# Optimization experiments

Hardware: AMD Instinct MI355X
Metric: run time of the kernel (lower is better)

Reference implementation:

```python
import jax, jax.numpy as jnp
import numpy as np


def reference(x, coef_ref, coef_qry):
    # x: [B, Hr, Wr, Hq, Wq] similarity tensor
    B, Hr, Wr, Hq, Wq = x.shape
    xr = x.reshape(B, Hr * Wr, Hq * Wq)  # [B, R, Q]
    # softmax over ref axis (axis=1) of coef_ref * (x - max over axis 1)
    xm_ref = xr - jnp.max(xr, axis=1, keepdims=True)
    conf_ref = jax.nn.softmax(coef_ref[0] * xm_ref, axis=1)
    # softmax over qry axis (axis=2) of coef_qry * (x - max over axis 2)
    xm_qry = xr - jnp.max(xr, axis=2, keepdims=True)
    conf_qry = jax.nn.softmax(coef_qry[0] * xm_qry, axis=2)
    confidence = jnp.sqrt(conf_ref * conf_qry)  # [B, R, Q]
    # top_k(k=1) over last axis + gather_nd of that value == max over axis 2
    values = jnp.max(confidence, axis=2)  # [B, R]
    return values.reshape(B, Hr, Wr, 1)


def setup_inputs() -> dict:
    key = jax.random.key(0)
    k1, = jax.random.split(key, 1)
    B, Hr, Wr, Hq, Wq = 16, 64, 64, 32, 32
    alpha = 10.0
    x = jax.random.normal(k1, (B, Hr, Wr, Hq, Wq), dtype=jnp.float32)
    coef_ref = jnp.full((1,), alpha, dtype=jnp.float32)
    coef_qry = jnp.full((1,), alpha, dtype=jnp.float32)
    return {"x": x, "coef_ref": coef_ref, "coef_qry": coef_qry}
```

## Files before the change

kernel.cpp:

```cpp
#include <hip/hip_runtime.h>
#include <math.h>
#include <stdint.h>


constexpr int B = 16;
constexpr int R = 4096;
constexpr int Q = 1024;
constexpr int CAP = 32;
#define DELTA 0.9f

__device__ __forceinline__ float wmax64(float v) {
#pragma unroll
    for (int o = 32; o; o >>= 1) v = fmaxf(v, __shfl_xor(v, o, 64));
    return v;
}
__device__ __forceinline__ float wsum64(float v) {
#pragma unroll
    for (int o = 32; o; o >>= 1) v += __shfl_xor(v, o, 64);
    return v;
}

__global__ __launch_bounds__(256) void qatm_pass1(
    const float* __restrict__ x,
    float* __restrict__ psum,
    float* __restrict__ rmArr,
    float* __restrict__ rsArr,
    uint32_t* __restrict__ cntArr,
    float2* __restrict__ cand,
    const float* __restrict__ coef_ref,
    const float* __restrict__ coef_qry)
{
    const int blk = blockIdx.x;
    const int b = blk >> 6, chunk = blk & 63;
    const int w = threadIdx.x >> 6, l = threadIdx.x & 63;
    const float ar = coef_ref[0], aq = coef_qry[0];
    const uint64_t lanemask = (1ull << l) - 1ull;

    const float4* xb = reinterpret_cast<const float4*>(x) +
                       ((size_t)b * R + (size_t)chunk * 64 + (size_t)w * 16) * (Q / 4);

    float4 cs0 = {0, 0, 0, 0}, cs1 = {0, 0, 0, 0}, cs2 = {0, 0, 0, 0}, cs3 = {0, 0, 0, 0};

#pragma unroll 4
    for (int rr = 0; rr < 16; ++rr) {
        const float4* xr = xb + (size_t)rr * (Q / 4);
        float4 v0 = xr[l], v1 = xr[64 + l], v2 = xr[128 + l], v3 = xr[192 + l];

        float lm = fmaxf(fmaxf(fmaxf(v0.x, v0.y), fmaxf(v0.z, v0.w)),
                   fmaxf(fmaxf(fmaxf(v1.x, v1.y), fmaxf(v1.z, v1.w)),
                   fmaxf(fmaxf(fmaxf(v2.x, v2.y), fmaxf(v2.z, v2.w)),
                         fmaxf(fmaxf(v3.x, v3.y), fmaxf(v3.z, v3.w)))));
        float rm = wmax64(lm);

        float rsum =
            __expf(aq * v0.x) + __expf(aq * v0.y) + __expf(aq * v0.z) + __expf(aq * v0.w) +
            __expf(aq * v1.x) + __expf(aq * v1.y) + __expf(aq * v1.z) + __expf(aq * v1.w) +
            __expf(aq * v2.x) + __expf(aq * v2.y) + __expf(aq * v2.z) + __expf(aq * v2.w) +
            __expf(aq * v3.x) + __expf(aq * v3.y) + __expf(aq * v3.z) + __expf(aq * v3.w);
        rsum = wsum64(rsum);

        cs0.x += __expf(ar * v0.x); cs0.y += __expf(ar * v0.y);
        cs0.z += __expf(ar * v0.z); cs0.w += __expf(ar * v0.w);
        cs1.x += __expf(ar * v1.x); cs1.y += __expf(ar * v1.y);
        cs1.z += __expf(ar * v1.z); cs1.w += __expf(ar * v1.w);
        cs2.x += __expf(ar * v2.x); cs2.y += __expf(ar * v2.y);
        cs2.z += __expf(ar * v2.z); cs2.w += __expf(ar * v2.w);
        cs3.x += __expf(ar * v3.x); cs3.y += __expf(ar * v3.y);
        cs3.z += __expf(ar * v3.z); cs3.w += __expf(ar * v3.w);

        const float th = rm - DELTA;
        uint32_t cnt = 0;
        const size_t grow = (size_t)b * R + (size_t)chunk * 64 + (size_t)w * 16 + rr;

#define CANDJ(val, colidx)                                                         \
        {                                                                          \
            bool p = (val) >= th;                                                  \
            uint64_t mk = __ballot(p);                                             \
            uint32_t off = cnt + (uint32_t)__popcll(mk & lanemask);                \
            if (p && off < CAP)                                                    \
                cand[grow * CAP + off] = make_float2((val), __uint_as_float(colidx)); \
            cnt += (uint32_t)__popcll(mk);                                         \
        }
        CANDJ(v0.x, 4 * l + 0) CANDJ(v0.y, 4 * l + 1) CANDJ(v0.z, 4 * l + 2) CANDJ(v0.w, 4 * l + 3)
        CANDJ(v1.x, 256 + 4 * l + 0) CANDJ(v1.y, 256 + 4 * l + 1) CANDJ(v1.z, 256 + 4 * l + 2) CANDJ(v1.w, 256 + 4 * l + 3)
        CANDJ(v2.x, 512 + 4 * l + 0) CANDJ(v2.y, 512 + 4 * l + 1) CANDJ(v2.z, 512 + 4 * l + 2) CANDJ(v2.w, 512 + 4 * l + 3)
        CANDJ(v3.x, 768 + 4 * l + 0) CANDJ(v3.y, 768 + 4 * l + 1) CANDJ(v3.z, 768 + 4 * l + 2) CANDJ(v3.w, 768 + 4 * l + 3)
#undef CANDJ

        if (l == 0) { rmArr[grow] = rm; rsArr[grow] = rsum; cntArr[grow] = cnt; }
    }

    __shared__ float4 sh[4][256];
    sh[w][l] = cs0; sh[w][64 + l] = cs1; sh[w][128 + l] = cs2; sh[w][192 + l] = cs3;
    __syncthreads();
    const int t = threadIdx.x;
    float4 a = sh[0][t], b4 = sh[1][t], c4 = sh[2][t], d4 = sh[3][t];
    float4 s;
    s.x = (a.x + b4.x) + (c4.x + d4.x);
    s.y = (a.y + b4.y) + (c4.y + d4.y);
    s.z = (a.z + b4.z) + (c4.z + d4.z);
    s.w = (a.w + b4.w) + (c4.w + d4.w);
    reinterpret_cast<float4*>(psum)[(size_t)blk * 256 + t] = s;
}

__global__ __launch_bounds__(1024) void qatm_combine(
    const float* __restrict__ psum, float* __restrict__ cvec,
    float* __restrict__ cminArr)
{
    const int b = blockIdx.x, q = threadIdx.x;
    float s = 0.f;
#pragma unroll 8
    for (int i = 0; i < 64; ++i) s += psum[(size_t)(b * 64 + i) * 1024 + q];
    const float c = __logf(s);
    cvec[b * 1024 + q] = c;
    __shared__ float red[1024];
    red[q] = c; __syncthreads();
    for (int st = 512; st > 0; st >>= 1) {
        if (q < st) red[q] = fminf(red[q], red[q + st]);
        __syncthreads();
    }
    if (q == 0) cminArr[b] = red[0];
}

__global__ __launch_bounds__(256) void qatm_select(
    const float* __restrict__ x, const float* __restrict__ cvec,
    const float* __restrict__ cminArr,
    const float* __restrict__ rmArr, const float* __restrict__ rsArr,
    const uint32_t* __restrict__ cntArr, const float2* __restrict__ cand,
    const float* __restrict__ coef_ref, const float* __restrict__ coef_qry,
    float* __restrict__ out)
{
    const int w = threadIdx.x >> 6, l = threadIdx.x & 63;
    const size_t row = (size_t)blockIdx.x * 4 + w;
    const int b = (int)(row >> 12);
    const float ar = coef_ref[0], aq = coef_qry[0], s2 = ar + aq;

    const uint32_t cnt = cntArr[row];
    const float rm = rmArr[row], rs = rsArr[row];

    float best = -INFINITY;
    bool fallback = (cnt > CAP);
    if (!fallback) {
        if (l < (int)cnt) {
            float2 cd = cand[row * CAP + l];
            int q = (int)__float_as_uint(cd.y);
            best = s2 * cd.x - cvec[((size_t)b << 10) + q];
        }
        best = wmax64(best);
        if (!(best >= s2 * (rm - DELTA) - cminArr[b])) fallback = true;
    }
    if (fallback) {
        const float4* xr = reinterpret_cast<const float4*>(x) + row * (Q / 4);
        const float4* cq = reinterpret_cast<const float4*>(cvec) + ((size_t)b * (Q / 4));
        best = -INFINITY;
#pragma unroll
        for (int it = 0; it < 4; ++it) {
            float4 v = xr[it * 64 + l], c4 = cq[it * 64 + l];
            best = fmaxf(best, fmaxf(fmaxf(s2 * v.x - c4.x, s2 * v.y - c4.y),
                                     fmaxf(s2 * v.z - c4.z, s2 * v.w - c4.w)));
        }
        best = wmax64(best);
    }
    if (l == 0) out[row] = __expf(0.5f * (best - __logf(rs)));
}

extern "C" void kernel_launch(void* const* d_in, const int* in_sizes, int n_in,
                              void* d_out, int out_size, void* d_ws, size_t ws_size,
                              hipStream_t stream) {
    const float* x = (const float*)d_in[0];
    const float* coef_ref = (const float*)d_in[1];
    const float* coef_qry = (const float*)d_in[2];
    float* out = (float*)d_out;

    char* ws = (char*)d_ws;
    float* psum = (float*)ws;                      size_t off = (size_t)B * 64 * 1024 * 4;
    float* cvec = (float*)(ws + off);              off += (size_t)B * 1024 * 4;
    float* cmin = (float*)(ws + off);              off += 256;
    float* rmA  = (float*)(ws + off);              off += (size_t)B * R * 4;
    float* rsA  = (float*)(ws + off);              off += (size_t)B * R * 4;
    uint32_t* cntA = (uint32_t*)(ws + off);        off += (size_t)B * R * 4;
    float2* cand = (float2*)(ws + off);

    qatm_pass1<<<B * 64, 256, 0, stream>>>(x, psum, rmA, rsA, cntA, cand,
                                           coef_ref, coef_qry);
    qatm_combine<<<B, 1024, 0, stream>>>(psum, cvec, cmin);
    qatm_select<<<(B * R) / 4, 256, 0, stream>>>(x, cvec, cmin, rmA, rsA, cntA, cand,
                                                 coef_ref, coef_qry, out);
}
```

Measured before the change: 100.3 us.

## Reuse exp when coefficients match, group candidates by float4, split combine kernel

When coef_ref equals coef_qry, pass1 computes the exponentials once and reuses them for both the column accumulators and the row sum, roughly halving exp work. Candidate selection now runs per float4 group instead of per element, so each row does 4 ballots instead of 16. Each candidate stores the whole float4 plus a group index, and select evaluates all four lanes. The combine step is split into a wide elementwise kernel plus a small min-reduction kernel, which adds one launch but uses many more blocks than the old 16. Group-level candidates can overflow the 16-slot cap more often and force the full-row fallback.

```diff
diff --git a/kernel.cpp b/kernel.cpp
--- a/kernel.cpp
+++ b/kernel.cpp
@@ -6,7 +6,7 @@
 constexpr int B = 16;
 constexpr int R = 4096;
 constexpr int Q = 1024;
-constexpr int CAP = 32;
+constexpr int CAP4 = 16;
 #define DELTA 0.9f
 
 __device__ __forceinline__ float wmax64(float v) {
@@ -18,6 +18,19 @@
 #pragma unroll
     for (int o = 32; o; o >>= 1) v += __shfl_xor(v, o, 64);
     return v;
+}
+__device__ __forceinline__ float max4(float4 v) {
+    return fmaxf(fmaxf(v.x, v.y), fmaxf(v.z, v.w));
+}
+__device__ __forceinline__ float sum4(float4 v) {
+    return (v.x + v.y) + (v.z + v.w);
+}
+__device__ __forceinline__ float4 exp4(float a, float4 v) {
+    return make_float4(__expf(a * v.x), __expf(a * v.y),
+                       __expf(a * v.z), __expf(a * v.w));
+}
+__device__ __forceinline__ void add4(float4& d, float4 s) {
+    d.x += s.x; d.y += s.y; d.z += s.z; d.w += s.w;
 }
 
 __global__ __launch_bounds__(256) void qatm_pass1(
@@ -26,7 +39,8 @@
     float* __restrict__ rmArr,
     float* __restrict__ rsArr,
     uint32_t* __restrict__ cntArr,
-    float2* __restrict__ cand,
+    float4* __restrict__ cand4,
+    uint32_t* __restrict__ candg,
     const float* __restrict__ coef_ref,
     const float* __restrict__ coef_qry)
 {
@@ -34,58 +48,53 @@
     const int b = blk >> 6, chunk = blk & 63;
     const int w = threadIdx.x >> 6, l = threadIdx.x & 63;
     const float ar = coef_ref[0], aq = coef_qry[0];
+    const bool same = (ar == aq);
     const uint64_t lanemask = (1ull << l) - 1ull;
 
-    const float4* xb = reinterpret_cast<const float4*>(x) +
-                       ((size_t)b * R + (size_t)chunk * 64 + (size_t)w * 16) * (Q / 4);
-
-    float4 cs0 = {0, 0, 0, 0}, cs1 = {0, 0, 0, 0}, cs2 = {0, 0, 0, 0}, cs3 = {0, 0, 0, 0};
-
-#pragma unroll 4
+    const size_t row0 = (size_t)b * R + (size_t)chunk * 64 + (size_t)w * 16;
+    const float4* xb = reinterpret_cast<const float4*>(x) + row0 * (Q / 4);
+
+    float4 cs0{0,0,0,0}, cs1{0,0,0,0}, cs2{0,0,0,0}, cs3{0,0,0,0};
+
     for (int rr = 0; rr < 16; ++rr) {
         const float4* xr = xb + (size_t)rr * (Q / 4);
         float4 v0 = xr[l], v1 = xr[64 + l], v2 = xr[128 + l], v3 = xr[192 + l];
 
-        float lm = fmaxf(fmaxf(fmaxf(v0.x, v0.y), fmaxf(v0.z, v0.w)),
-                   fmaxf(fmaxf(fmaxf(v1.x, v1.y), fmaxf(v1.z, v1.w)),
-                   fmaxf(fmaxf(fmaxf(v2.x, v2.y), fmaxf(v2.z, v2.w)),
-                         fmaxf(fmaxf(v3.x, v3.y), fmaxf(v3.z, v3.w)))));
-        float rm = wmax64(lm);
-
-        float rsum =
-            __expf(aq * v0.x) + __expf(aq * v0.y) + __expf(aq * v0.z) + __expf(aq * v0.w) +
-            __expf(aq * v1.x) + __expf(aq * v1.y) + __expf(aq * v1.z) + __expf(aq * v1.w) +
-            __expf(aq * v2.x) + __expf(aq * v2.y) + __expf(aq * v2.z) + __expf(aq * v2.w) +
-            __expf(aq * v3.x) + __expf(aq * v3.y) + __expf(aq * v3.z) + __expf(aq * v3.w);
+        float g0 = max4(v0), g1 = max4(v1), g2 = max4(v2), g3 = max4(v3);
+        float rm = wmax64(fmaxf(fmaxf(g0, g1), fmaxf(g2, g3)));
+
+        float4 e0 = exp4(ar, v0), e1 = exp4(ar, v1),
+               e2 = exp4(ar, v2), e3 = exp4(ar, v3);
+        add4(cs0, e0); add4(cs1, e1); add4(cs2, e2); add4(cs3, e3);
+
+        float rsum;
+        if (same) {
+            rsum = (sum4(e0) + sum4(e1)) + (sum4(e2) + sum4(e3));
+        } else {
+            rsum = (sum4(exp4(aq, v0)) + sum4(exp4(aq, v1))) +
+                   (sum4(exp4(aq, v2)) + sum4(exp4(aq, v3)));
+        }
         rsum = wsum64(rsum);
-
-        cs0.x += __expf(ar * v0.x); cs0.y += __expf(ar * v0.y);
-        cs0.z += __expf(ar * v0.z); cs0.w += __expf(ar * v0.w);
-        cs1.x += __expf(ar * v1.x); cs1.y += __expf(ar * v1.y);
-        cs1.z += __expf(ar * v1.z); cs1.w += __expf(ar * v1.w);
-        cs2.x += __expf(ar * v2.x); cs2.y += __expf(ar * v2.y);
-        cs2.z += __expf(ar * v2.z); cs2.w += __expf(ar * v2.w);
-        cs3.x += __expf(ar * v3.x); cs3.y += __expf(ar * v3.y);
-        cs3.z += __expf(ar * v3.z); cs3.w += __expf(ar * v3.w);
 
         const float th = rm - DELTA;
         uint32_t cnt = 0;
-        const size_t grow = (size_t)b * R + (size_t)chunk * 64 + (size_t)w * 16 + rr;
-
-#define CANDJ(val, colidx)                                                         \
-        {                                                                          \
-            bool p = (val) >= th;                                                  \
-            uint64_t mk = __ballot(p);                                             \
-            uint32_t off = cnt + (uint32_t)__popcll(mk & lanemask);                \
-            if (p && off < CAP)                                                    \
-                cand[grow * CAP + off] = make_float2((val), __uint_as_float(colidx)); \
-            cnt += (uint32_t)__popcll(mk);                                         \
-        }
-        CANDJ(v0.x, 4 * l + 0) CANDJ(v0.y, 4 * l + 1) CANDJ(v0.z, 4 * l + 2) CANDJ(v0.w, 4 * l + 3)
-        CANDJ(v1.x, 256 + 4 * l + 0) CANDJ(v1.y, 256 + 4 * l + 1) CANDJ(v1.z, 256 + 4 * l + 2) CANDJ(v1.w, 256 + 4 * l + 3)
-        CANDJ(v2.x, 512 + 4 * l + 0) CANDJ(v2.y, 512 + 4 * l + 1) CANDJ(v2.z, 512 + 4 * l + 2) CANDJ(v2.w, 512 + 4 * l + 3)
-        CANDJ(v3.x, 768 + 4 * l + 0) CANDJ(v3.y, 768 + 4 * l + 1) CANDJ(v3.z, 768 + 4 * l + 2) CANDJ(v3.w, 768 + 4 * l + 3)
-#undef CANDJ
+        const size_t grow = row0 + rr;
+        float4* cbase = cand4 + grow * CAP4;
+        uint32_t* gbase = candg + grow * CAP4;
+
+#define CAND4(gm, vec, gi)                                                  \
+        {                                                                   \
+            bool p = (gm) >= th;                                            \
+            uint64_t mk = __ballot(p);                                      \
+            uint32_t off = cnt + (uint32_t)__popcll(mk & lanemask);         \
+            if (p && off < CAP4) { cbase[off] = (vec); gbase[off] = (gi); } \
+            cnt += (uint32_t)__popcll(mk);                                  \
+        }
+        CAND4(g0, v0, (uint32_t)l)
+        CAND4(g1, v1, (uint32_t)(64 + l))
+        CAND4(g2, v2, (uint32_t)(128 + l))
+        CAND4(g3, v3, (uint32_t)(192 + l))
+#undef CAND4
 
         if (l == 0) { rmArr[grow] = rm; rsArr[grow] = rsum; cntArr[grow] = cnt; }
     }
@@ -103,30 +112,36 @@
     reinterpret_cast<float4*>(psum)[(size_t)blk * 256 + t] = s;
 }
 
-__global__ __launch_bounds__(1024) void qatm_combine(
-    const float* __restrict__ psum, float* __restrict__ cvec,
-    float* __restrict__ cminArr)
-{
-    const int b = blockIdx.x, q = threadIdx.x;
+__global__ __launch_bounds__(256) void qatm_combine(
+    const float* __restrict__ psum, float* __restrict__ cvec)
+{
+    const int tid = blockIdx.x * 256 + threadIdx.x;
+    const int b = tid >> 10, q = tid & (Q - 1);
     float s = 0.f;
 #pragma unroll 8
     for (int i = 0; i < 64; ++i) s += psum[(size_t)(b * 64 + i) * 1024 + q];
-    const float c = __logf(s);
-    cvec[b * 1024 + q] = c;
-    __shared__ float red[1024];
-    red[q] = c; __syncthreads();
-    for (int st = 512; st > 0; st >>= 1) {
-        if (q < st) red[q] = fminf(red[q], red[q + st]);
-        __syncthreads();
-    }
-    if (q == 0) cminArr[b] = red[0];
+    cvec[tid] = __logf(s);
+}
+
+__global__ __launch_bounds__(256) void qatm_cmin(
+    const float* __restrict__ cvec, float* __restrict__ cminArr)
+{
+    const int b = blockIdx.x, t = threadIdx.x;
+    float4 c = reinterpret_cast<const float4*>(cvec)[b * 256 + t];
+    float m = fminf(fminf(c.x, c.y), fminf(c.z, c.w));
+    m = -wmax64(-m);
+    __shared__ float sh[4];
+    if ((t & 63) == 0) sh[t >> 6] = m;
+    __syncthreads();
+    if (t == 0) cminArr[b] = fminf(fminf(sh[0], sh[1]), fminf(sh[2], sh[3]));
 }
 
 __global__ __launch_bounds__(256) void qatm_select(
     const float* __restrict__ x, const float* __restrict__ cvec,
     const float* __restrict__ cminArr,
     const float* __restrict__ rmArr, const float* __restrict__ rsArr,
-    const uint32_t* __restrict__ cntArr, const float2* __restrict__ cand,
+    const uint32_t* __restrict__ cntArr,
+    const float4* __restrict__ cand4, const uint32_t* __restrict__ candg,
     const float* __restrict__ coef_ref, const float* __restrict__ coef_qry,
     float* __restrict__ out)
 {
@@ -139,25 +154,27 @@
     const float rm = rmArr[row], rs = rsArr[row];
 
     float best = -INFINITY;
-    bool fallback = (cnt > CAP);
+    bool fallback = (cnt > CAP4);
     if (!fallback) {
         if (l < (int)cnt) {
-            float2 cd = cand[row * CAP + l];
-            int q = (int)__float_as_uint(cd.y);
-            best = s2 * cd.x - cvec[((size_t)b << 10) + q];
+            float4 v = cand4[row * CAP4 + l];
+            uint32_t g = candg[row * CAP4 + l];
+            float4 c = reinterpret_cast<const float4*>(cvec)[((size_t)b << 8) + g];
+            best = fmaxf(fmaxf(s2 * v.x - c.x, s2 * v.y - c.y),
+                         fmaxf(s2 * v.z - c.z, s2 * v.w - c.w));
         }
         best = wmax64(best);
         if (!(best >= s2 * (rm - DELTA) - cminArr[b])) fallback = true;
     }
     if (fallback) {
         const float4* xr = reinterpret_cast<const float4*>(x) + row * (Q / 4);
-        const float4* cq = reinterpret_cast<const float4*>(cvec) + ((size_t)b * (Q / 4));
+        const float4* cq = reinterpret_cast<const float4*>(cvec) + ((size_t)b << 8);
         best = -INFINITY;
 #pragma unroll
         for (int it = 0; it < 4; ++it) {
-            float4 v = xr[it * 64 + l], c4 = cq[it * 64 + l];
-            best = fmaxf(best, fmaxf(fmaxf(s2 * v.x - c4.x, s2 * v.y - c4.y),
-                                     fmaxf(s2 * v.z - c4.z, s2 * v.w - c4.w)));
+            float4 v = xr[it * 64 + l], c = cq[it * 64 + l];
+            best = fmaxf(best, fmaxf(fmaxf(s2 * v.x - c.x, s2 * v.y - c.y),
+                                     fmaxf(s2 * v.z - c.z, s2 * v.w - c.w)));
         }
         best = wmax64(best);
     }
@@ -173,17 +190,20 @@
     float* out = (float*)d_out;
 
     char* ws = (char*)d_ws;
-    float* psum = (float*)ws;                      size_t off = (size_t)B * 64 * 1024 * 4;
-    float* cvec = (float*)(ws + off);              off += (size_t)B * 1024 * 4;
-    float* cmin = (float*)(ws + off);              off += 256;
-    float* rmA  = (float*)(ws + off);              off += (size_t)B * R * 4;
-    float* rsA  = (float*)(ws + off);              off += (size_t)B * R * 4;
-    uint32_t* cntA = (uint32_t*)(ws + off);        off += (size_t)B * R * 4;
-    float2* cand = (float2*)(ws + off);
-
-    qatm_pass1<<<B * 64, 256, 0, stream>>>(x, psum, rmA, rsA, cntA, cand,
+    size_t off = 0;
+    float*    psum  = (float*)(ws + off);    off += (size_t)B * 64 * 1024 * 4;
+    float4*   cand4 = (float4*)(ws + off);   off += (size_t)B * R * CAP4 * 16;
+    uint32_t* candg = (uint32_t*)(ws + off); off += (size_t)B * R * CAP4 * 4;
+    float*    cvec  = (float*)(ws + off);    off += (size_t)B * Q * 4;
+    float*    rmA   = (float*)(ws + off);    off += (size_t)B * R * 4;
+    float*    rsA   = (float*)(ws + off);    off += (size_t)B * R * 4;
+    uint32_t* cntA  = (uint32_t*)(ws + off); off += (size_t)B * R * 4;
+    float*    cmin  = (float*)(ws + off);
+
+    qatm_pass1<<<B * 64, 256, 0, stream>>>(x, psum, rmA, rsA, cntA, cand4, candg,
                                            coef_ref, coef_qry);
-    qatm_combine<<<B, 1024, 0, stream>>>(psum, cvec, cmin);
-    qatm_select<<<(B * R) / 4, 256, 0, stream>>>(x, cvec, cmin, rmA, rsA, cntA, cand,
-                                                 coef_ref, coef_qry, out);
-}
+    qatm_combine<<<(B * Q) / 256, 256, 0, stream>>>(psum, cvec);
+    qatm_cmin<<<B, 256, 0, stream>>>(cvec, cmin);
+    qatm_select<<<(B * R) / 4, 256, 0, stream>>>(x, cvec, cmin, rmA, rsA, cntA,
+                                                 cand4, candg, coef_ref, coef_qry, out);
+}
```

After: 85.67 us. 1.17x faster.
